# Optimization experiments

Measured on AMD Instinct MI355X. Metric: run time of the kernel, lower is better.

The kernel has to match this reference:

```python
import jax, jax.numpy as jnp
import numpy as np

P, D_IN, RANK, D_OUT, N = 64, 1024, 64, 1024, 4096


def setup_inputs() -> dict:
    key = jax.random.key(0)
    k1, k2, k3, k4, k5 = jax.random.split(key, 5)
    x = jax.random.normal(k1, (N, D_IN), dtype=jnp.float32)
    pids = jax.random.randint(k2, (N,), 0, P, dtype=jnp.int64)
    U = jax.random.normal(k3, (P, D_IN, RANK), dtype=jnp.float32) * 0.02
    V = jax.random.normal(k4, (P, RANK, D_OUT), dtype=jnp.float32) * 0.02
    bias = jax.random.normal(k5, (D_OUT,), dtype=jnp.float32)
    return {"x": x, "pids": pids, "U": U, "V": V, "bias": bias}


def reference(x, pids, U, V, bias):
    # Equivalent to: for each token n, out[n] = x[n] @ U[pids[n]] @ V[pids[n]] + bias
    # Computed as dense grouped GEMM over all partitions, then row-select by pid
    # (identical math to the masked per-partition loop in the torch module).
    h = jnp.einsum('nd,pdr->pnr', x, U)        # [P, N, R]
    o = jnp.einsum('pnr,pro->pno', h, V)       # [P, N, D_out]
    out = o[pids, jnp.arange(x.shape[0])] + bias  # select each token's own partition
    return out
```

## Files before the change

### kernel.cpp

```cpp
#include <hip/hip_runtime.h>
#include <hip/hip_bf16.h>

#define NP     64
#define D_IN   1024
#define RANK   64
#define D_OUT  1024
#define NTOK   4096
#define TM     64
#define BK     64
#define MT     128
#define KS     8
#define KW     (D_IN / KS)
#define OW     128
#define OSPLIT (D_OUT / OW)
#define LDSTR  72

typedef __bf16 bf16x8 __attribute__((ext_vector_type(8)));
typedef float  f32x4  __attribute__((ext_vector_type(4)));

__device__ __forceinline__ unsigned short f2bf(float f) {
    unsigned u = __builtin_bit_cast(unsigned, f);
    u += 0x7FFFu + ((u >> 16) & 1u);
    return (unsigned short)(u >> 16);
}
__device__ __forceinline__ float bf2f(unsigned short s) {
    unsigned u = (unsigned)s << 16;
    return __builtin_bit_cast(float, u);
}
__device__ __forceinline__ bf16x8 pack8(float4 a, float4 b) {
    union { bf16x8 v; unsigned short s[8]; } r;
    r.s[0] = f2bf(a.x); r.s[1] = f2bf(a.y); r.s[2] = f2bf(a.z); r.s[3] = f2bf(a.w);
    r.s[4] = f2bf(b.x); r.s[5] = f2bf(b.y); r.s[6] = f2bf(b.z); r.s[7] = f2bf(b.w);
    return r.v;
}

__global__ void bucket_kernel(const int* __restrict__ pids, int* __restrict__ meta) {
    __shared__ int counts[NP];
    __shared__ int cursor[NP];
    int tid = threadIdx.x;
    if (tid < NP) counts[tid] = 0;
    __syncthreads();
    for (int i = tid; i < NTOK; i += 256)
        atomicAdd(&counts[pids[i] & (NP - 1)], 1);
    __syncthreads();
    if (tid < 64) {
        int c = counts[tid];
        int ntp = (c + TM - 1) >> 6;
        int sc = c, st = ntp;
        for (int d = 1; d < 64; d <<= 1) {
            int vc = __shfl_up(sc, d);
            int vt = __shfl_up(st, d);
            if (tid >= d) { sc += vc; st += vt; }
        }
        int cbase = sc - c;
        int tb    = st - ntp;
        cursor[tid] = cbase;
        for (int t = 0; t < ntp; ++t) {
            int idx = tb + t;
            meta[16 + idx]  = tid;
            meta[144 + idx] = cbase + t * TM;
            int rem = c - t * TM;
            meta[272 + idx] = rem < TM ? rem : TM;
        }
        if (tid == 63) meta[0] = st;
    }
    __syncthreads();
    int* bucket = meta + 512;
    for (int i = tid; i < NTOK; i += 256) {
        int p = pids[i] & (NP - 1);
        int pos = atomicAdd(&cursor[p], 1);
        bucket[pos] = i;
    }
}

__global__ __launch_bounds__(256, 4) void h_kernel(
    const float* __restrict__ x, const float* __restrict__ U,
    const int* __restrict__ meta, unsigned short* __restrict__ Hpart)
{
    __shared__ __align__(16) unsigned short Us[RANK][LDSTR];
    __shared__ int toks[TM];

    int tile = blockIdx.x >> 3;
    int ks   = blockIdx.x & 7;
    int nt = meta[0];
    if (tile >= nt) return;
    int p   = meta[16 + tile];
    int off = meta[144 + tile];
    int len = meta[272 + tile];

    int tid  = threadIdx.x;
    int lane = tid & 63;
    int w    = tid >> 6;
    int l15  = lane & 15;
    int l4   = lane >> 4;

    const int* bucket = meta + 512;
    if (tid < TM) toks[tid] = (tid < len) ? bucket[off + tid] : -1;
    __syncthreads();

    int myrow = w * 16 + l15;
    int t = toks[myrow];
    bool valid = (t >= 0);
    const float* xrow = x + (size_t)(valid ? t : 0) * D_IN;
    const float* Up = U + (size_t)p * D_IN * RANK;

    int kbeg = ks * KW;

    float4 z{0,0,0,0};
    float4 c0a=z,c0b=z,c0c=z,c0d=z,c1a=z,c1b=z,c1c=z,c1d=z;
    if (valid) {
        const float* xp = xrow + kbeg + l4 * 8;
        c0a = *reinterpret_cast<const float4*>(xp);
        c0b = *reinterpret_cast<const float4*>(xp + 4);
        c0c = *reinterpret_cast<const float4*>(xp + 32);
        c0d = *reinterpret_cast<const float4*>(xp + 36);
        c1a = *reinterpret_cast<const float4*>(xp + 64);
        c1b = *reinterpret_cast<const float4*>(xp + 68);
        c1c = *reinterpret_cast<const float4*>(xp + 96);
        c1d = *reinterpret_cast<const float4*>(xp + 100);
    }

    f32x4 acc[4] = {};

    {
        int kk = tid >> 2;
        int q  = (tid & 3) * 16;
        const float* up = Up + (size_t)(kbeg + kk) * RANK + q;
#pragma unroll
        for (int i = 0; i < 4; ++i) {
            float4 v = *reinterpret_cast<const float4*>(up + i * 4);
            int r = q + i * 4;
            Us[r + 0][kk] = f2bf(v.x);
            Us[r + 1][kk] = f2bf(v.y);
            Us[r + 2][kk] = f2bf(v.z);
            Us[r + 3][kk] = f2bf(v.w);
        }
    }
    __syncthreads();
    {
        bf16x8 a0 = pack8(c0a, c0b);
        bf16x8 a1 = pack8(c0c, c0d);
#pragma unroll
        for (int k2 = 0; k2 < 2; ++k2) {
            int kof = k2 * 32 + l4 * 8;
            bf16x8 a = k2 ? a1 : a0;
#pragma unroll
            for (int ni = 0; ni < 4; ++ni) {
                bf16x8 b = *reinterpret_cast<const bf16x8*>(&Us[ni * 16 + l15][kof]);
                acc[ni] = __builtin_amdgcn_mfma_f32_16x16x32_bf16(a, b, acc[ni], 0, 0, 0);
            }
        }
    }
    __syncthreads();
    {
        int kk = tid >> 2;
        int q  = (tid & 3) * 16;
        const float* up = Up + (size_t)(kbeg + BK + kk) * RANK + q;
#pragma unroll
        for (int i = 0; i < 4; ++i) {
            float4 v = *reinterpret_cast<const float4*>(up + i * 4);
            int r = q + i * 4;
            Us[r + 0][kk] = f2bf(v.x);
            Us[r + 1][kk] = f2bf(v.y);
            Us[r + 2][kk] = f2bf(v.z);
            Us[r + 3][kk] = f2bf(v.w);
        }
    }
    __syncthreads();
    {
        bf16x8 a0 = pack8(c1a, c1b);
        bf16x8 a1 = pack8(c1c, c1d);
#pragma unroll
        for (int k2 = 0; k2 < 2; ++k2) {
            int kof = k2 * 32 + l4 * 8;
            bf16x8 a = k2 ? a1 : a0;
#pragma unroll
            for (int ni = 0; ni < 4; ++ni) {
                bf16x8 b = *reinterpret_cast<const bf16x8*>(&Us[ni * 16 + l15][kof]);
                acc[ni] = __builtin_amdgcn_mfma_f32_16x16x32_bf16(a, b, acc[ni], 0, 0, 0);
            }
        }
    }

    unsigned short* hp = Hpart + ((size_t)ks * MT + tile) * (TM * RANK);
#pragma unroll
    for (int ni = 0; ni < 4; ++ni)
#pragma unroll
        for (int j = 0; j < 4; ++j) {
            int row = w * 16 + l4 * 4 + j;
            int col = ni * 16 + l15;
            hp[row * RANK + col] = f2bf(acc[ni][j]);
        }
}

__global__ __launch_bounds__(256, 4) void hsum_kernel(
    const int* __restrict__ meta, const unsigned short* __restrict__ Hpart,
    unsigned short* __restrict__ Hbf)
{
    int tile = blockIdx.x >> 1;
    int half = blockIdx.x & 1;
    if (tile >= meta[0]) return;
    int e = half * 2048 + threadIdx.x * 8;

    float s[8] = {};
#pragma unroll
    for (int ks = 0; ks < KS; ++ks) {
        union { int4 i4; unsigned short u[8]; } v;
        v.i4 = *reinterpret_cast<const int4*>(
            &Hpart[((size_t)ks * MT + tile) * (TM * RANK) + e]);
#pragma unroll
        for (int j = 0; j < 8; ++j) s[j] += bf2f(v.u[j]);
    }
    union { int4 i4; unsigned short u[8]; } o;
#pragma unroll
    for (int j = 0; j < 8; ++j) o.u[j] = f2bf(s[j]);
    *reinterpret_cast<int4*>(&Hbf[(size_t)tile * (TM * RANK) + e]) = o.i4;
}

__global__ __launch_bounds__(256, 4) void o_kernel(
    const float* __restrict__ V, const float* __restrict__ bias,
    const int* __restrict__ meta, const unsigned short* __restrict__ Hbf,
    float* __restrict__ out)
{
    __shared__ __align__(16) unsigned short Vs[OW][LDSTR];
    __shared__ int toks[TM];

    int tile = blockIdx.x >> 3;
    int oc   = (blockIdx.x & 7) * OW;
    int nt = meta[0];
    if (tile >= nt) return;
    int p   = meta[16 + tile];
    int off = meta[144 + tile];
    int len = meta[272 + tile];

    int tid  = threadIdx.x;
    int lane = tid & 63;
    int w    = tid >> 6;
    int l15  = lane & 15;
    int l4   = lane >> 4;

    const int* bucket = meta + 512;
    if (tid < TM) toks[tid] = (tid < len) ? bucket[off + tid] : -1;

    const float* Vp = V + (size_t)p * RANK * D_OUT;
    {
        int o4 = (tid & 31) * 4;
        int rb = tid >> 5;
#pragma unroll
        for (int pass = 0; pass < 8; ++pass) {
            int r = pass * 8 + rb;
            float4 v = *reinterpret_cast<const float4*>(&Vp[(size_t)r * D_OUT + oc + o4]);
            Vs[o4 + 0][r] = f2bf(v.x);
            Vs[o4 + 1][r] = f2bf(v.y);
            Vs[o4 + 2][r] = f2bf(v.z);
            Vs[o4 + 3][r] = f2bf(v.w);
        }
    }
    __syncthreads();

    const unsigned short* Hrow = Hbf + (size_t)tile * (TM * RANK) + (w * 16 + l15) * RANK;

    f32x4 acc[8] = {};
#pragma unroll
    for (int k2 = 0; k2 < 2; ++k2) {
        int kof = k2 * 32 + l4 * 8;
        bf16x8 a = *reinterpret_cast<const bf16x8*>(Hrow + kof);
#pragma unroll
        for (int ni = 0; ni < 8; ++ni) {
            bf16x8 b = *reinterpret_cast<const bf16x8*>(&Vs[ni * 16 + l15][kof]);
            acc[ni] = __builtin_amdgcn_mfma_f32_16x16x32_bf16(a, b, acc[ni], 0, 0, 0);
        }
    }

    int r0 = w * 16 + l4 * 4;
    int t0 = toks[r0 + 0], t1 = toks[r0 + 1], t2 = toks[r0 + 2], t3 = toks[r0 + 3];
#pragma unroll
    for (int ni = 0; ni < 8; ++ni) {
        int col = oc + ni * 16 + l15;
        float bv = bias[col];
        if (r0 + 0 < len) out[(size_t)t0 * D_OUT + col] = acc[ni][0] + bv;
        if (r0 + 1 < len) out[(size_t)t1 * D_OUT + col] = acc[ni][1] + bv;
        if (r0 + 2 < len) out[(size_t)t2 * D_OUT + col] = acc[ni][2] + bv;
        if (r0 + 3 < len) out[(size_t)t3 * D_OUT + col] = acc[ni][3] + bv;
    }
}

extern "C" void kernel_launch(void* const* d_in, const int* in_sizes, int n_in,
                              void* d_out, int out_size, void* d_ws, size_t ws_size,
                              hipStream_t stream) {
    const float* x    = (const float*)d_in[0];
    const int*   pids = (const int*)d_in[1];
    const float* U    = (const float*)d_in[2];
    const float* V    = (const float*)d_in[3];
    const float* bias = (const float*)d_in[4];
    float* out = (float*)d_out;

    int* meta = (int*)d_ws;
    unsigned short* Hbf = (unsigned short*)((char*)d_ws + 65536);
    unsigned short* Hpart = (unsigned short*)((char*)d_ws + 65536
                            + (size_t)MT * TM * RANK * sizeof(unsigned short));

    bucket_kernel<<<1, 256, 0, stream>>>(pids, meta);
    h_kernel<<<MT * KS, 256, 0, stream>>>(x, U, meta, Hpart);
    hsum_kernel<<<MT * 2, 256, 0, stream>>>(meta, Hpart, Hbf);
    o_kernel<<<MT * OSPLIT, 256, 0, stream>>>(V, bias, meta, Hbf, out);
}
```

Before: 42.33 us.

## Fuse split-K reduction into h_kernel via last-block atomic counter and double-buffer U

Removes the separate hsum kernel launch. Each h_kernel block increments a per-tile counter after writing its partial, and the last of the KS blocks sums all partials into Hbf. U staging is double-buffered in shared memory so the second chunk's global loads overlap the first chunk's MFMAs, which also drops a barrier. o_kernel now issues its H loads before staging V. The cost is extra thread fences and atomics, and a serialized reduction tail in whichever block finishes last.

```diff
diff --git a/kernel.cpp b/kernel.cpp
--- a/kernel.cpp
+++ b/kernel.cpp
@@ -12,8 +12,8 @@
 #define KS     8
 #define KW     (D_IN / KS)
 #define OW     128
-#define OSPLIT (D_OUT / OW)
 #define LDSTR  72
+#define CTRO   4608
 
 typedef __bf16 bf16x8 __attribute__((ext_vector_type(8)));
 typedef float  f32x4  __attribute__((ext_vector_type(4)));
@@ -38,6 +38,7 @@
     __shared__ int counts[NP];
     __shared__ int cursor[NP];
     int tid = threadIdx.x;
+    if (tid < MT) meta[CTRO + tid] = 0;
     if (tid < NP) counts[tid] = 0;
     __syncthreads();
     for (int i = tid; i < NTOK; i += 256)
@@ -75,10 +76,12 @@
 
 __global__ __launch_bounds__(256, 4) void h_kernel(
     const float* __restrict__ x, const float* __restrict__ U,
-    const int* __restrict__ meta, unsigned short* __restrict__ Hpart)
+    int* __restrict__ meta, unsigned short* __restrict__ Hpart,
+    unsigned short* __restrict__ Hbf)
 {
-    __shared__ __align__(16) unsigned short Us[RANK][LDSTR];
+    __shared__ __align__(16) unsigned short Us[2][RANK][LDSTR];
     __shared__ int toks[TM];
+    __shared__ int amlast;
 
     int tile = blockIdx.x >> 3;
     int ks   = blockIdx.x & 7;
@@ -105,6 +108,8 @@
     const float* Up = U + (size_t)p * D_IN * RANK;
 
     int kbeg = ks * KW;
+    int kk = tid >> 2;
+    int q  = (tid & 3) * 16;
 
     float4 z{0,0,0,0};
     float4 c0a=z,c0b=z,c0c=z,c0d=z,c1a=z,c1b=z,c1c=z,c1d=z;
@@ -123,20 +128,28 @@
     f32x4 acc[4] = {};
 
     {
-        int kk = tid >> 2;
-        int q  = (tid & 3) * 16;
         const float* up = Up + (size_t)(kbeg + kk) * RANK + q;
 #pragma unroll
         for (int i = 0; i < 4; ++i) {
             float4 v = *reinterpret_cast<const float4*>(up + i * 4);
             int r = q + i * 4;
-            Us[r + 0][kk] = f2bf(v.x);
-            Us[r + 1][kk] = f2bf(v.y);
-            Us[r + 2][kk] = f2bf(v.z);
-            Us[r + 3][kk] = f2bf(v.w);
-        }
-    }
-    __syncthreads();
+            Us[0][r + 0][kk] = f2bf(v.x);
+            Us[0][r + 1][kk] = f2bf(v.y);
+            Us[0][r + 2][kk] = f2bf(v.z);
+            Us[0][r + 3][kk] = f2bf(v.w);
+        }
+    }
+    __syncthreads();
+
+    float4 u10, u11, u12, u13;
+    {
+        const float* up = Up + (size_t)(kbeg + BK + kk) * RANK + q;
+        u10 = *reinterpret_cast<const float4*>(up);
+        u11 = *reinterpret_cast<const float4*>(up + 4);
+        u12 = *reinterpret_cast<const float4*>(up + 8);
+        u13 = *reinterpret_cast<const float4*>(up + 12);
+    }
+
     {
         bf16x8 a0 = pack8(c0a, c0b);
         bf16x8 a1 = pack8(c0c, c0d);
@@ -146,27 +159,25 @@
             bf16x8 a = k2 ? a1 : a0;
 #pragma unroll
             for (int ni = 0; ni < 4; ++ni) {
-                bf16x8 b = *reinterpret_cast<const bf16x8*>(&Us[ni * 16 + l15][kof]);
+                bf16x8 b = *reinterpret_cast<const bf16x8*>(&Us[0][ni * 16 + l15][kof]);
                 acc[ni] = __builtin_amdgcn_mfma_f32_16x16x32_bf16(a, b, acc[ni], 0, 0, 0);
             }
         }
     }
-    __syncthreads();
-    {
-        int kk = tid >> 2;
-        int q  = (tid & 3) * 16;
-        const float* up = Up + (size_t)(kbeg + BK + kk) * RANK + q;
+
+    {
+        float4 vv[4] = {u10, u11, u12, u13};
 #pragma unroll
         for (int i = 0; i < 4; ++i) {
-            float4 v = *reinterpret_cast<const float4*>(up + i * 4);
             int r = q + i * 4;
-            Us[r + 0][kk] = f2bf(v.x);
-            Us[r + 1][kk] = f2bf(v.y);
-            Us[r + 2][kk] = f2bf(v.z);
-            Us[r + 3][kk] = f2bf(v.w);
-        }
-    }
-    __syncthreads();
+            Us[1][r + 0][kk] = f2bf(vv[i].x);
+            Us[1][r + 1][kk] = f2bf(vv[i].y);
+            Us[1][r + 2][kk] = f2bf(vv[i].z);
+            Us[1][r + 3][kk] = f2bf(vv[i].w);
+        }
+    }
+    __syncthreads();
+
     {
         bf16x8 a0 = pack8(c1a, c1b);
         bf16x8 a1 = pack8(c1c, c1d);
@@ -176,7 +187,7 @@
             bf16x8 a = k2 ? a1 : a0;
 #pragma unroll
             for (int ni = 0; ni < 4; ++ni) {
-                bf16x8 b = *reinterpret_cast<const bf16x8*>(&Us[ni * 16 + l15][kof]);
+                bf16x8 b = *reinterpret_cast<const bf16x8*>(&Us[1][ni * 16 + l15][kof]);
                 acc[ni] = __builtin_amdgcn_mfma_f32_16x16x32_bf16(a, b, acc[ni], 0, 0, 0);
             }
         }
@@ -191,30 +202,32 @@
             int col = ni * 16 + l15;
             hp[row * RANK + col] = f2bf(acc[ni][j]);
         }
-}
-
-__global__ __launch_bounds__(256, 4) void hsum_kernel(
-    const int* __restrict__ meta, const unsigned short* __restrict__ Hpart,
-    unsigned short* __restrict__ Hbf)
-{
-    int tile = blockIdx.x >> 1;
-    int half = blockIdx.x & 1;
-    if (tile >= meta[0]) return;
-    int e = half * 2048 + threadIdx.x * 8;
-
-    float s[8] = {};
-#pragma unroll
-    for (int ks = 0; ks < KS; ++ks) {
-        union { int4 i4; unsigned short u[8]; } v;
-        v.i4 = *reinterpret_cast<const int4*>(
-            &Hpart[((size_t)ks * MT + tile) * (TM * RANK) + e]);
-#pragma unroll
-        for (int j = 0; j < 8; ++j) s[j] += bf2f(v.u[j]);
-    }
-    union { int4 i4; unsigned short u[8]; } o;
-#pragma unroll
-    for (int j = 0; j < 8; ++j) o.u[j] = f2bf(s[j]);
-    *reinterpret_cast<int4*>(&Hbf[(size_t)tile * (TM * RANK) + e]) = o.i4;
+
+    __threadfence();
+    __syncthreads();
+    if (tid == 0)
+        amlast = (atomicAdd(&meta[CTRO + tile], 1) == KS - 1);
+    __syncthreads();
+    if (!amlast) return;
+    __threadfence();
+
+    int e = tid * 16;
+    float s[16] = {};
+#pragma unroll
+    for (int k = 0; k < KS; ++k) {
+        const unsigned short* pp = Hpart + ((size_t)k * MT + tile) * (TM * RANK) + e;
+        union { int4 i4; unsigned short u[8]; } v0, v1;
+        v0.i4 = *reinterpret_cast<const int4*>(pp);
+        v1.i4 = *reinterpret_cast<const int4*>(pp + 8);
+#pragma unroll
+        for (int j = 0; j < 8; ++j) { s[j] += bf2f(v0.u[j]); s[8 + j] += bf2f(v1.u[j]); }
+    }
+    union { int4 i4; unsigned short u[8]; } o0, o1;
+#pragma unroll
+    for (int j = 0; j < 8; ++j) { o0.u[j] = f2bf(s[j]); o1.u[j] = f2bf(s[8 + j]); }
+    unsigned short* hb = Hbf + (size_t)tile * (TM * RANK) + e;
+    *reinterpret_cast<int4*>(hb)     = o0.i4;
+    *reinterpret_cast<int4*>(hb + 8) = o1.i4;
 }
 
 __global__ __launch_bounds__(256, 4) void o_kernel(
@@ -239,6 +252,10 @@
     int l15  = lane & 15;
     int l4   = lane >> 4;
 
+    const unsigned short* Hrow = Hbf + (size_t)tile * (TM * RANK) + (w * 16 + l15) * RANK;
+    bf16x8 a0 = *reinterpret_cast<const bf16x8*>(Hrow + l4 * 8);
+    bf16x8 a1 = *reinterpret_cast<const bf16x8*>(Hrow + 32 + l4 * 8);
+
     const int* bucket = meta + 512;
     if (tid < TM) toks[tid] = (tid < len) ? bucket[off + tid] : -1;
 
@@ -258,13 +275,11 @@
     }
     __syncthreads();
 
-    const unsigned short* Hrow = Hbf + (size_t)tile * (TM * RANK) + (w * 16 + l15) * RANK;
-
     f32x4 acc[8] = {};
 #pragma unroll
     for (int k2 = 0; k2 < 2; ++k2) {
         int kof = k2 * 32 + l4 * 8;
-        bf16x8 a = *reinterpret_cast<const bf16x8*>(Hrow + kof);
+        bf16x8 a = k2 ? a1 : a0;
 #pragma unroll
         for (int ni = 0; ni < 8; ++ni) {
             bf16x8 b = *reinterpret_cast<const bf16x8*>(&Vs[ni * 16 + l15][kof]);
@@ -301,7 +316,6 @@
                             + (size_t)MT * TM * RANK * sizeof(unsigned short));
 
     bucket_kernel<<<1, 256, 0, stream>>>(pids, meta);
-    h_kernel<<<MT * KS, 256, 0, stream>>>(x, U, meta, Hpart);
-    hsum_kernel<<<MT * 2, 256, 0, stream>>>(meta, Hpart, Hbf);
-    o_kernel<<<MT * OSPLIT, 256, 0, stream>>>(V, bias, meta, Hbf, out);
-}
+    h_kernel<<<MT * KS, 256, 0, stream>>>(x, U, meta, Hpart, Hbf);
+    o_kernel<<<MT * 8, 256, 0, stream>>>(V, bias, meta, Hbf, out);
+}
```

Result: slower. 154.3 us (+264.4%).
